# Kernel optimization log

Hardware: AMD Instinct MI355X
Metric: run time of the kernel (lower is better)

Reference implementation:

```python
import jax, jax.numpy as jnp
import numpy as np

DIM = 1024
HEADS = 16
HEAD_DIM = DIM // HEADS


def setup_inputs() -> dict:
    key = jax.random.key(0)
    ks = jax.random.split(key, 9)
    s = 1.0 / np.sqrt(DIM)
    return {
        "x": jax.random.normal(ks[0], (2, 2048, DIM), dtype=jnp.float32),
        "Wq": jax.random.normal(ks[1], (DIM, DIM), dtype=jnp.float32) * s,
        "bq": jnp.zeros((DIM,), dtype=jnp.float32),
        "Wk": jax.random.normal(ks[2], (DIM, DIM), dtype=jnp.float32) * s,
        "bk": jnp.zeros((DIM,), dtype=jnp.float32),
        "Wv": jax.random.normal(ks[3], (DIM, DIM), dtype=jnp.float32) * s,
        "bv": jnp.zeros((DIM,), dtype=jnp.float32),
        "Wo": jax.random.normal(ks[4], (DIM, DIM), dtype=jnp.float32) * s,
        "bo": jnp.zeros((DIM,), dtype=jnp.float32),
    }


def reference(x, Wq, bq, Wk, bk, Wv, bv, Wo, bo):
    B, S, D = x.shape
    H, Dh = HEADS, HEAD_DIM

    def split_heads(t):  # (B,S,D) -> (B,H,S,Dh)
        return t.reshape(B, S, H, Dh).transpose(0, 2, 1, 3)

    q = split_heads(x @ Wq + bq)
    k = split_heads(x @ Wk + bk)
    v = split_heads(x @ Wv + bv)

    scores = jnp.einsum("bhsd,bhtd->bhst", q, k) / np.sqrt(Dh).astype(x.dtype)
    attn = jax.nn.softmax(scores, axis=-1)
    ctx = jnp.einsum("bhst,bhtd->bhsd", attn, v)
    ctx = ctx.transpose(0, 2, 1, 3).reshape(B, S, D)
    return ctx @ Wo + bo
```

## Files before the change

kernel.cpp:

```cpp
#include <hip/hip_runtime.h>
#include <hip/hip_bf16.h>
#include <cstdint>

typedef __bf16 bf16;
typedef __bf16 bf16x8 __attribute__((ext_vector_type(8)));
typedef float f32x4 __attribute__((ext_vector_type(4)));
typedef float f32x8 __attribute__((ext_vector_type(8)));
typedef float f32x16 __attribute__((ext_vector_type(16)));

#define DIM   1024
#define SEQ   2048
#define BATCH 2
#define HEADS 16
#define HDIM  64

#define QSCALE 0.1803368801111204f

__device__ __forceinline__ void gload_lds16(const void* g, void* l) {
    __builtin_amdgcn_global_load_lds(
        (const __attribute__((address_space(1))) void*)g,
        (__attribute__((address_space(3))) void*)l,
        16, 0, 0);
}

__device__ __forceinline__ uint32_t pkbf(float a, float b) {
    union { bf16 h[2]; uint32_t u; } t;
    t.h[0] = (bf16)a; t.h[1] = (bf16)b;
    return t.u;
}

#define LO8(v)  __builtin_shufflevector(v, v, 0, 1, 2, 3, 4, 5, 6, 7)
#define HI8(v)  __builtin_shufflevector(v, v, 8, 9, 10, 11, 12, 13, 14, 15)
#define LO4(v)  __builtin_shufflevector(v, v, 0, 1, 2, 3)
#define HI4(v)  __builtin_shufflevector(v, v, 4, 5, 6, 7)

__global__ __launch_bounds__(256) void cvt_wt_kernel(const float* __restrict__ Wq,
                                                     const float* __restrict__ Wk,
                                                     const float* __restrict__ Wv,
                                                     const float* __restrict__ Wo,
                                                     bf16* __restrict__ Wt) {
    int z = blockIdx.z;
    const float* W = (z == 0) ? Wq : (z == 1) ? Wk : (z == 2) ? Wv : Wo;
    bf16* out = Wt + (size_t)z * DIM * DIM;
    int w = threadIdx.x >> 6, lane = threadIdx.x & 63;
    int n  = blockIdx.x * 64 + lane;
    int kb = blockIdx.y * 32 + w * 8;
    bf16x8 o;
#pragma unroll
    for (int j = 0; j < 8; ++j)
        o[j] = (bf16)W[(size_t)(kb + j) * DIM + n];
    *(bf16x8*)(out + (size_t)n * DIM + kb) = o;
}

template <int MODE>
__global__ __launch_bounds__(256) void gemm128_kernel(
        const void* __restrict__ Ap,
        const void* __restrict__ A2p,
        const float* __restrict__ lb,
        const bf16* __restrict__ WtB,
        const float* __restrict__ b0,
        const float* __restrict__ b1,
        const float* __restrict__ b2,
        void* __restrict__ outp) {
    constexpr int K = DIM;
    int z = (MODE == 0) ? blockIdx.z : 0;
    const bf16* Bt = WtB + (size_t)z * DIM * DIM;
    const float* bias = (MODE == 0) ? ((z == 0) ? b0 : (z == 1) ? b1 : b2) : b0;

    int m0 = blockIdx.y * 128, n0 = blockIdx.x * 128;
    int tid = threadIdx.x;
    int w = tid >> 6, lane = tid & 63, l15 = lane & 15, l4 = lane >> 4;
    int wr = (w >> 1) * 64, wc = (w & 1) * 64;

    __shared__ __align__(16) bf16 As[128 * 32];
    __shared__ __align__(16) bf16 Bs[128 * 32];

    int arow = tid >> 1, acol = (tid & 1) * 16;
    int r = m0 + arow;
    const float* asrc = (MODE == 0)
        ? (const float*)Ap + (size_t)r * K + acol : nullptr;

    f32x4 acc[4][4] = {};

    for (int k0 = 0; k0 < K; k0 += 32) {
#pragma unroll
        for (int rr = 0; rr < 2; ++rr) {
            int c = rr * 256 + tid;
            gload_lds16(Bt + (size_t)(n0 + (c >> 2)) * K + k0 + (c & 3) * 8, &Bs[c * 8]);
        }
        if constexpr (MODE == 0) {
            const float4* s4 = (const float4*)(asrc + k0);
            float4 f0 = s4[0], f1 = s4[1], f2 = s4[2], f3 = s4[3];
            bf16x8 e0, e1;
            e0[0] = (bf16)f0.x; e0[1] = (bf16)f0.y; e0[2] = (bf16)f0.z; e0[3] = (bf16)f0.w;
            e0[4] = (bf16)f1.x; e0[5] = (bf16)f1.y; e0[6] = (bf16)f1.z; e0[7] = (bf16)f1.w;
            e1[0] = (bf16)f2.x; e1[1] = (bf16)f2.y; e1[2] = (bf16)f2.z; e1[3] = (bf16)f2.w;
            e1[4] = (bf16)f3.x; e1[5] = (bf16)f3.y; e1[6] = (bf16)f3.z; e1[7] = (bf16)f3.w;
            *(bf16x8*)&As[arow * 32 + acol]     = e0;
            *(bf16x8*)&As[arow * 32 + acol + 8] = e1;
        } else {
            int s = r & (SEQ - 1), bbq = r >> 11;
            int hb2 = bbq * HEADS + ((k0 + acol) >> 6);
            float linv = 1.0f / (lb[(size_t)hb2 * SEQ + s]
                               + lb[((size_t)BATCH * HEADS + hb2) * SEQ + s]);
            const bf16* p0 = (const bf16*)Ap  + (size_t)r * DIM + k0 + acol;
            const bf16* p1 = (const bf16*)A2p + (size_t)r * DIM + k0 + acol;
            bf16x8 u0 = *(const bf16x8*)p0, u1 = *(const bf16x8*)(p0 + 8);
            bf16x8 t0 = *(const bf16x8*)p1, t1 = *(const bf16x8*)(p1 + 8);
            bf16x8 e0, e1;
#pragma unroll
            for (int i2 = 0; i2 < 8; ++i2) {
                e0[i2] = (bf16)(((float)u0[i2] + (float)t0[i2]) * linv);
                e1[i2] = (bf16)(((float)u1[i2] + (float)t1[i2]) * linv);
            }
            *(bf16x8*)&As[arow * 32 + acol]     = e0;
            *(bf16x8*)&As[arow * 32 + acol + 8] = e1;
        }
        __syncthreads();
        bf16x8 af[4], bfr[4];
#pragma unroll
        for (int m = 0; m < 4; ++m)
            af[m] = *(const bf16x8*)&As[(wr + m * 16 + l15) * 32 + l4 * 8];
#pragma unroll
        for (int n = 0; n < 4; ++n)
            bfr[n] = *(const bf16x8*)&Bs[(wc + n * 16 + l15) * 32 + l4 * 8];
#pragma unroll
        for (int m = 0; m < 4; ++m)
#pragma unroll
            for (int n = 0; n < 4; ++n)
                acc[m][n] = __builtin_amdgcn_mfma_f32_16x16x32_bf16(
                    af[m], bfr[n], acc[m][n], 0, 0, 0);
        __syncthreads();
    }

    float oscale = (MODE == 0 && z == 0) ? QSCALE : 1.0f;
#pragma unroll
    for (int n = 0; n < 4; ++n) {
        int col = n0 + wc + n * 16 + l15;
        float bv = bias[col];
#pragma unroll
        for (int m = 0; m < 4; ++m) {
            int rowb = m0 + wr + m * 16 + l4 * 4;
            if (MODE == 1) {
                float* out = (float*)outp;
#pragma unroll
                for (int i = 0; i < 4; ++i)
                    out[(size_t)(rowb + i) * DIM + col] = acc[m][n][i] + bv;
            } else if (z == 0) {
                bf16* out = (bf16*)outp;
                int h = col >> 6, d = col & 63;
#pragma unroll
                for (int i = 0; i < 4; ++i) {
                    int row = rowb + i;
                    int bb = row >> 11, s = row & 2047;
                    out[(((size_t)(bb * HEADS + h)) * SEQ + s) * HDIM + d] =
                        (bf16)((acc[m][n][i] + bv) * oscale);
                }
            } else if (z == 1) {
                char* out = (char*)outp + (size_t)(BATCH * HEADS * SEQ * HDIM) * 2;
                int h = col >> 6, d = col & 63;
                int ks = d >> 4, lbase = ((d >> 3) & 1) * 32, e = d & 7;
#pragma unroll
                for (int i = 0; i < 4; ++i) {
                    int row = rowb + i;
                    int bb = row >> 11, s = row & 2047;
                    int hb2 = bb * HEADS + h;
                    size_t off = (size_t)(hb2 * 64 + (s >> 5)) * 4096
                                 + ks * 1024 + ((s & 31) + lbase) * 16 + e * 2;
                    *(bf16*)(out + off) = (bf16)(acc[m][n][i] + bv);
                }
            } else {
                char* out = (char*)outp + (size_t)2 * (BATCH * HEADS * SEQ * HDIM) * 2;
                int h = col >> 6, d = col & 63;
                int dblk = d >> 5;
                int bb = rowb >> 11, s0 = rowb & 2047;
                int hb2 = bb * HEADS + h;
                int lane2 = (d & 31) + 32 * ((s0 >> 3) & 1);
                size_t off = (size_t)(hb2 * 64 + (s0 >> 5)) * 4096
                             + (dblk * 2 + ((s0 >> 4) & 1)) * 1024
                             + lane2 * 16 + (s0 & 7) * 2;
                union { bf16 hh[4]; ushort4 v; } pk;
#pragma unroll
                for (int i = 0; i < 4; ++i) pk.hh[i] = (bf16)(acc[m][n][i] + bv);
                *(ushort4*)(out + off) = pk.v;
            }
        }
    }
}

__global__ __launch_bounds__(256) void attn_kernel(const bf16* __restrict__ Q,
                                                   const bf16* __restrict__ Kf,
                                                   const bf16* __restrict__ Vf,
                                                   bf16* __restrict__ op0,
                                                   bf16* __restrict__ op1,
                                                   float* __restrict__ lbuf) {
    int bid = blockIdx.x;
    int xcd = bid & 7, i = bid >> 3;
    int hb  = xcd * 4 + (i >> 4);
    int rem = i & 15;
    int q0  = (rem >> 1) * 256;
    int si  = rem & 1;
    int bb = hb >> 4, h = hb & 15;
    int tid = threadIdx.x, w = tid >> 6, lane = tid & 63;
    int l31 = lane & 31, hi = lane >> 5;

    const bf16* Qh = Q + (size_t)hb * SEQ * HDIM;
    const char* kj = (const char*)Kf + (size_t)(hb * 64 + si * 32) * 4096 + lane * 16;
    const char* vj = (const char*)Vf + (size_t)(hb * 64 + si * 32) * 4096 + lane * 16;

    int qrowA = q0 + w * 64 + l31;
    int qrowB = qrowA + 32;
    bf16x8 qfA[4], qfB[4];
#pragma unroll
    for (int ks = 0; ks < 4; ++ks) {
        qfA[ks] = *(const bf16x8*)&Qh[(size_t)qrowA * HDIM + ks * 16 + hi * 8];
        qfB[ks] = *(const bf16x8*)&Qh[(size_t)qrowB * HDIM + ks * 16 + hi * 8];
    }

    f32x16 oA0 = {}, oA1 = {}, oB0 = {}, oB1 = {};
    float lA = 0.f, lB = 0.f;

    for (int j = 0; j < 32; ++j) {
        bf16x8 k0 = *(const bf16x8*)(kj);
        bf16x8 k1 = *(const bf16x8*)(kj + 1024);
        bf16x8 k2 = *(const bf16x8*)(kj + 2048);
        bf16x8 k3 = *(const bf16x8*)(kj + 3072);
        kj += 4096;

        f32x16 sA = {}, sB = {};
        __builtin_amdgcn_s_setprio(1);
        sA = __builtin_amdgcn_mfma_f32_32x32x16_bf16(k0, qfA[0], sA, 0, 0, 0);
        sA = __builtin_amdgcn_mfma_f32_32x32x16_bf16(k1, qfA[1], sA, 0, 0, 0);
        sA = __builtin_amdgcn_mfma_f32_32x32x16_bf16(k2, qfA[2], sA, 0, 0, 0);
        sA = __builtin_amdgcn_mfma_f32_32x32x16_bf16(k3, qfA[3], sA, 0, 0, 0);
        sB = __builtin_amdgcn_mfma_f32_32x32x16_bf16(k0, qfB[0], sB, 0, 0, 0);
        sB = __builtin_amdgcn_mfma_f32_32x32x16_bf16(k1, qfB[1], sB, 0, 0, 0);
        sB = __builtin_amdgcn_mfma_f32_32x32x16_bf16(k2, qfB[2], sB, 0, 0, 0);
        sB = __builtin_amdgcn_mfma_f32_32x32x16_bf16(k3, qfB[3], sB, 0, 0, 0);
        __builtin_amdgcn_s_setprio(0);

        bf16x8 v0 = *(const bf16x8*)(vj);
        bf16x8 v1 = *(const bf16x8*)(vj + 1024);
        bf16x8 v2 = *(const bf16x8*)(vj + 2048);
        bf16x8 v3 = *(const bf16x8*)(vj + 3072);
        vj += 4096;

#pragma unroll
        for (int r = 0; r < 16; ++r)
            sA[r] = __builtin_amdgcn_exp2f(sA[r]);
        {
            f32x8 a8 = LO8(sA) + HI8(sA);
            f32x4 a4 = LO4(a8) + HI4(a8);
            lA += (a4[0] + a4[1]) + (a4[2] + a4[3]);
        }
        bf16x8 paA0, paA1;
        {
            uint32_t w0 = pkbf(sA[0], sA[1]), w1 = pkbf(sA[2], sA[3]);
            uint32_t w2 = pkbf(sA[4], sA[5]), w3 = pkbf(sA[6], sA[7]);
            asm("v_permlane32_swap_b32 %0, %1" : "+v"(w0), "+v"(w2));
            asm("v_permlane32_swap_b32 %0, %1" : "+v"(w1), "+v"(w3));
            union { uint32_t u[4]; bf16x8 v; } t2;
            t2.u[0] = w0; t2.u[1] = w1; t2.u[2] = w2; t2.u[3] = w3;
            paA0 = t2.v;
            uint32_t u0 = pkbf(sA[8], sA[9]),   u1 = pkbf(sA[10], sA[11]);
            uint32_t u2 = pkbf(sA[12], sA[13]), u3 = pkbf(sA[14], sA[15]);
            asm("v_permlane32_swap_b32 %0, %1" : "+v"(u0), "+v"(u2));
            asm("v_permlane32_swap_b32 %0, %1" : "+v"(u1), "+v"(u3));
            union { uint32_t u[4]; bf16x8 v; } t3;
            t3.u[0] = u0; t3.u[1] = u1; t3.u[2] = u2; t3.u[3] = u3;
            paA1 = t3.v;
        }
        __builtin_amdgcn_s_setprio(1);
        oA0 = __builtin_amdgcn_mfma_f32_32x32x16_bf16(v0, paA0, oA0, 0, 0, 0);
        oA0 = __builtin_amdgcn_mfma_f32_32x32x16_bf16(v1, paA1, oA0, 0, 0, 0);
        oA1 = __builtin_amdgcn_mfma_f32_32x32x16_bf16(v2, paA0, oA1, 0, 0, 0);
        oA1 = __builtin_amdgcn_mfma_f32_32x32x16_bf16(v3, paA1, oA1, 0, 0, 0);
        __builtin_amdgcn_s_setprio(0);

#pragma unroll
        for (int r = 0; r < 16; ++r)
            sB[r] = __builtin_amdgcn_exp2f(sB[r]);
        {
            f32x8 a8 = LO8(sB) + HI8(sB);
            f32x4 a4 = LO4(a8) + HI4(a8);
            lB += (a4[0] + a4[1]) + (a4[2] + a4[3]);
        }
        bf16x8 paB0, paB1;
        {
            uint32_t w0 = pkbf(sB[0], sB[1]), w1 = pkbf(sB[2], sB[3]);
            uint32_t w2 = pkbf(sB[4], sB[5]), w3 = pkbf(sB[6], sB[7]);
            asm("v_permlane32_swap_b32 %0, %1" : "+v"(w0), "+v"(w2));
            asm("v_permlane32_swap_b32 %0, %1" : "+v"(w1), "+v"(w3));
            union { uint32_t u[4]; bf16x8 v; } t2;
            t2.u[0] = w0; t2.u[1] = w1; t2.u[2] = w2; t2.u[3] = w3;
            paB0 = t2.v;
            uint32_t u0 = pkbf(sB[8], sB[9]),   u1 = pkbf(sB[10], sB[11]);
            uint32_t u2 = pkbf(sB[12], sB[13]), u3 = pkbf(sB[14], sB[15]);
            asm("v_permlane32_swap_b32 %0, %1" : "+v"(u0), "+v"(u2));
            asm("v_permlane32_swap_b32 %0, %1" : "+v"(u1), "+v"(u3));
            union { uint32_t u[4]; bf16x8 v; } t3;
            t3.u[0] = u0; t3.u[1] = u1; t3.u[2] = u2; t3.u[3] = u3;
            paB1 = t3.v;
        }
        __builtin_amdgcn_s_setprio(1);
        oB0 = __builtin_amdgcn_mfma_f32_32x32x16_bf16(v0, paB0, oB0, 0, 0, 0);
        oB0 = __builtin_amdgcn_mfma_f32_32x32x16_bf16(v1, paB1, oB0, 0, 0, 0);
        oB1 = __builtin_amdgcn_mfma_f32_32x32x16_bf16(v2, paB0, oB1, 0, 0, 0);
        oB1 = __builtin_amdgcn_mfma_f32_32x32x16_bf16(v3, paB1, oB1, 0, 0, 0);
        __builtin_amdgcn_s_setprio(0);
    }

    lA += __shfl_xor(lA, 32);
    lB += __shfl_xor(lB, 32);
    bf16* op = si ? op1 : op0;
    if (hi == 0) {
        lbuf[((size_t)si * BATCH * HEADS + hb) * SEQ + qrowA] = lA;
        lbuf[((size_t)si * BATCH * HEADS + hb) * SEQ + qrowB] = lB;
    }
    size_t baseA = ((size_t)bb * SEQ + qrowA) * DIM + h * HDIM;
    size_t baseB = ((size_t)bb * SEQ + qrowB) * DIM + h * HDIM;
#pragma unroll
    for (int g = 0; g < 4; ++g) {
        int dh0 = 8 * g + 4 * hi;
        union { bf16 hh[4]; ushort4 u; } a0, a1, b0, b1;
#pragma unroll
        for (int i = 0; i < 4; ++i) {
            a0.hh[i] = (bf16)oA0[4 * g + i];
            a1.hh[i] = (bf16)oA1[4 * g + i];
            b0.hh[i] = (bf16)oB0[4 * g + i];
            b1.hh[i] = (bf16)oB1[4 * g + i];
        }
        *(ushort4*)&op[baseA + dh0]      = a0.u;
        *(ushort4*)&op[baseA + 32 + dh0] = a1.u;
        *(ushort4*)&op[baseB + dh0]      = b0.u;
        *(ushort4*)&op[baseB + 32 + dh0] = b1.u;
    }
}

extern "C" void kernel_launch(void* const* d_in, const int* in_sizes, int n_in,
                              void* d_out, int out_size, void* d_ws, size_t ws_size,
                              hipStream_t stream) {
    const float* x  = (const float*)d_in[0];
    const float* Wq = (const float*)d_in[1];
    const float* bq = (const float*)d_in[2];
    const float* Wk = (const float*)d_in[3];
    const float* bk = (const float*)d_in[4];
    const float* Wv = (const float*)d_in[5];
    const float* bv = (const float*)d_in[6];
    const float* Wo = (const float*)d_in[7];
    const float* bo = (const float*)d_in[8];

    char* ws = (char*)d_ws;
    bf16*  op0  = (bf16*)ws;
    bf16*  Wt   = (bf16*)(ws + (8u  << 20));
    float* lbuf = (float*)(ws + (8u  << 20));
    bf16*  Qb   = (bf16*)(ws + (16u << 20));
    bf16*  Kf   = (bf16*)(ws + (24u << 20));
    bf16*  Vf   = (bf16*)(ws + (32u << 20));
    bf16*  op1  = (bf16*)(ws + (40u << 20));

    cvt_wt_kernel<<<dim3(16, 32, 4), 256, 0, stream>>>(Wq, Wk, Wv, Wo, Wt);
    gemm128_kernel<0><<<dim3(8, 32, 3), 256, 0, stream>>>(
        x, nullptr, nullptr, Wt, bq, bk, bv, (void*)Qb);
    attn_kernel<<<512, 256, 0, stream>>>(Qb, Kf, Vf, op0, op1, lbuf);
    gemm128_kernel<1><<<dim3(8, 32, 1), 256, 0, stream>>>(
        op0, op1, lbuf, Wt + (size_t)3 * DIM * DIM, bo, bo, bo, (void*)d_out);
}
```

Baseline: 149.5 us.

## Split attention KV range four ways and merge partials in separate kernel

The attention kernel is templated on the number of KV splits. When the workspace is large enough it launches twice as many blocks, each covering a quarter of the keys and writing its own partial output and row sum. A new elementwise merge kernel adds the partials and normalises them into a single bf16 context buffer. The output projection GEMM can then load its A operand straight into LDS with global_load_lds instead of combining and normalising partials itself. This trades an extra kernel launch and an extra pass over the partial buffers for more attention parallelism and a simpler GEMM prologue.

```diff
diff --git a/kernel.cpp b/kernel.cpp
--- a/kernel.cpp
+++ b/kernel.cpp
@@ -55,8 +55,6 @@
 template <int MODE>
 __global__ __launch_bounds__(256) void gemm128_kernel(
         const void* __restrict__ Ap,
-        const void* __restrict__ A2p,
-        const float* __restrict__ lb,
         const bf16* __restrict__ WtB,
         const float* __restrict__ b0,
         const float* __restrict__ b1,
@@ -76,9 +74,8 @@
     __shared__ __align__(16) bf16 Bs[128 * 32];
 
     int arow = tid >> 1, acol = (tid & 1) * 16;
-    int r = m0 + arow;
     const float* asrc = (MODE == 0)
-        ? (const float*)Ap + (size_t)r * K + acol : nullptr;
+        ? (const float*)Ap + (size_t)(m0 + arow) * K + acol : nullptr;
 
     f32x4 acc[4][4] = {};
 
@@ -99,22 +96,12 @@
             *(bf16x8*)&As[arow * 32 + acol]     = e0;
             *(bf16x8*)&As[arow * 32 + acol + 8] = e1;
         } else {
-            int s = r & (SEQ - 1), bbq = r >> 11;
-            int hb2 = bbq * HEADS + ((k0 + acol) >> 6);
-            float linv = 1.0f / (lb[(size_t)hb2 * SEQ + s]
-                               + lb[((size_t)BATCH * HEADS + hb2) * SEQ + s]);
-            const bf16* p0 = (const bf16*)Ap  + (size_t)r * DIM + k0 + acol;
-            const bf16* p1 = (const bf16*)A2p + (size_t)r * DIM + k0 + acol;
-            bf16x8 u0 = *(const bf16x8*)p0, u1 = *(const bf16x8*)(p0 + 8);
-            bf16x8 t0 = *(const bf16x8*)p1, t1 = *(const bf16x8*)(p1 + 8);
-            bf16x8 e0, e1;
-#pragma unroll
-            for (int i2 = 0; i2 < 8; ++i2) {
-                e0[i2] = (bf16)(((float)u0[i2] + (float)t0[i2]) * linv);
-                e1[i2] = (bf16)(((float)u1[i2] + (float)t1[i2]) * linv);
+            const bf16* A = (const bf16*)Ap;
+#pragma unroll
+            for (int rr = 0; rr < 2; ++rr) {
+                int c = rr * 256 + tid;
+                gload_lds16(A + (size_t)(m0 + (c >> 2)) * K + k0 + (c & 3) * 8, &As[c * 8]);
             }
-            *(bf16x8*)&As[arow * 32 + acol]     = e0;
-            *(bf16x8*)&As[arow * 32 + acol + 8] = e1;
         }
         __syncthreads();
         bf16x8 af[4], bfr[4];
@@ -188,25 +175,31 @@
     }
 }
 
+template <int NSPLIT>
 __global__ __launch_bounds__(256) void attn_kernel(const bf16* __restrict__ Q,
                                                    const bf16* __restrict__ Kf,
                                                    const bf16* __restrict__ Vf,
                                                    bf16* __restrict__ op0,
                                                    bf16* __restrict__ op1,
+                                                   bf16* __restrict__ op2,
+                                                   bf16* __restrict__ op3,
                                                    float* __restrict__ lbuf) {
+    constexpr int BPH = 8 * NSPLIT;
     int bid = blockIdx.x;
     int xcd = bid & 7, i = bid >> 3;
-    int hb  = xcd * 4 + (i >> 4);
-    int rem = i & 15;
-    int q0  = (rem >> 1) * 256;
-    int si  = rem & 1;
+    int hb  = xcd * 4 + i / BPH;
+    int rem = i % BPH;
+    int q0  = (rem / NSPLIT) * 256;
+    int si  = rem % NSPLIT;
     int bb = hb >> 4, h = hb & 15;
     int tid = threadIdx.x, w = tid >> 6, lane = tid & 63;
     int l31 = lane & 31, hi = lane >> 5;
 
     const bf16* Qh = Q + (size_t)hb * SEQ * HDIM;
-    const char* kj = (const char*)Kf + (size_t)(hb * 64 + si * 32) * 4096 + lane * 16;
-    const char* vj = (const char*)Vf + (size_t)(hb * 64 + si * 32) * 4096 + lane * 16;
+    const char* kj = (const char*)Kf
+        + (size_t)(hb * 64 + si * (64 / NSPLIT)) * 4096 + lane * 16;
+    const char* vj = (const char*)Vf
+        + (size_t)(hb * 64 + si * (64 / NSPLIT)) * 4096 + lane * 16;
 
     int qrowA = q0 + w * 64 + l31;
     int qrowB = qrowA + 32;
@@ -220,7 +213,8 @@
     f32x16 oA0 = {}, oA1 = {}, oB0 = {}, oB1 = {};
     float lA = 0.f, lB = 0.f;
 
-    for (int j = 0; j < 32; ++j) {
+    constexpr int NJ = SEQ / NSPLIT / 32;
+    for (int j = 0; j < NJ; ++j) {
         bf16x8 k0 = *(const bf16x8*)(kj);
         bf16x8 k1 = *(const bf16x8*)(kj + 1024);
         bf16x8 k2 = *(const bf16x8*)(kj + 2048);
@@ -312,7 +306,7 @@
 
     lA += __shfl_xor(lA, 32);
     lB += __shfl_xor(lB, 32);
-    bf16* op = si ? op1 : op0;
+    bf16* op = (si == 0) ? op0 : (si == 1) ? op1 : (si == 2) ? op2 : op3;
     if (hi == 0) {
         lbuf[((size_t)si * BATCH * HEADS + hb) * SEQ + qrowA] = lA;
         lbuf[((size_t)si * BATCH * HEADS + hb) * SEQ + qrowB] = lB;
@@ -324,17 +318,54 @@
         int dh0 = 8 * g + 4 * hi;
         union { bf16 hh[4]; ushort4 u; } a0, a1, b0, b1;
 #pragma unroll
-        for (int i = 0; i < 4; ++i) {
-            a0.hh[i] = (bf16)oA0[4 * g + i];
-            a1.hh[i] = (bf16)oA1[4 * g + i];
-            b0.hh[i] = (bf16)oB0[4 * g + i];
-            b1.hh[i] = (bf16)oB1[4 * g + i];
+        for (int i2 = 0; i2 < 4; ++i2) {
+            a0.hh[i2] = (bf16)oA0[4 * g + i2];
+            a1.hh[i2] = (bf16)oA1[4 * g + i2];
+            b0.hh[i2] = (bf16)oB0[4 * g + i2];
+            b1.hh[i2] = (bf16)oB1[4 * g + i2];
         }
         *(ushort4*)&op[baseA + dh0]      = a0.u;
         *(ushort4*)&op[baseA + 32 + dh0] = a1.u;
         *(ushort4*)&op[baseB + dh0]      = b0.u;
         *(ushort4*)&op[baseB + 32 + dh0] = b1.u;
     }
+}
+
+template <int NSPLIT>
+__global__ __launch_bounds__(256) void merge_kernel(const bf16* __restrict__ op0,
+                                                    const bf16* __restrict__ op1,
+                                                    const bf16* __restrict__ op2,
+                                                    const bf16* __restrict__ op3,
+                                                    const float* __restrict__ lbuf,
+                                                    bf16* __restrict__ ctx) {
+    int idx = blockIdx.x * 256 + threadIdx.x;
+    size_t e8 = (size_t)idx * 8;
+    int row = (int)(e8 >> 10);
+    int d   = (int)(e8 & 1023);
+    int h = d >> 6;
+    int bb = row >> 11, s = row & 2047;
+    int hb = bb * HEADS + h;
+    float lsum = lbuf[(size_t)hb * SEQ + s]
+               + lbuf[((size_t)BATCH * HEADS + hb) * SEQ + s];
+    if constexpr (NSPLIT == 4)
+        lsum += lbuf[((size_t)2 * BATCH * HEADS + hb) * SEQ + s]
+              + lbuf[((size_t)3 * BATCH * HEADS + hb) * SEQ + s];
+    float inv = 1.0f / lsum;
+    bf16x8 a = *(const bf16x8*)&op0[e8];
+    bf16x8 b = *(const bf16x8*)&op1[e8];
+    float acc[8];
+#pragma unroll
+    for (int i = 0; i < 8; ++i) acc[i] = (float)a[i] + (float)b[i];
+    if constexpr (NSPLIT == 4) {
+        bf16x8 c = *(const bf16x8*)&op2[e8];
+        bf16x8 dd = *(const bf16x8*)&op3[e8];
+#pragma unroll
+        for (int i = 0; i < 8; ++i) acc[i] += (float)c[i] + (float)dd[i];
+    }
+    bf16x8 o;
+#pragma unroll
+    for (int i = 0; i < 8; ++i) o[i] = (bf16)(acc[i] * inv);
+    *(bf16x8*)&ctx[e8] = o;
 }
 
 extern "C" void kernel_launch(void* const* d_in, const int* in_sizes, int n_in,
@@ -358,11 +389,21 @@
     bf16*  Kf   = (bf16*)(ws + (24u << 20));
     bf16*  Vf   = (bf16*)(ws + (32u << 20));
     bf16*  op1  = (bf16*)(ws + (40u << 20));
+    bf16*  op2  = (bf16*)(ws + (48u << 20));
+    bf16*  op3  = (bf16*)(ws + (56u << 20));
 
     cvt_wt_kernel<<<dim3(16, 32, 4), 256, 0, stream>>>(Wq, Wk, Wv, Wo, Wt);
     gemm128_kernel<0><<<dim3(8, 32, 3), 256, 0, stream>>>(
-        x, nullptr, nullptr, Wt, bq, bk, bv, (void*)Qb);
-    attn_kernel<<<512, 256, 0, stream>>>(Qb, Kf, Vf, op0, op1, lbuf);
+        x, Wt, bq, bk, bv, (void*)Qb);
+
+    if (ws_size >= (64ull << 20)) {
+        attn_kernel<4><<<1024, 256, 0, stream>>>(Qb, Kf, Vf, op0, op1, op2, op3, lbuf);
+        merge_kernel<4><<<2048, 256, 0, stream>>>(op0, op1, op2, op3, lbuf, op0);
+    } else {
+        attn_kernel<2><<<512, 256, 0, stream>>>(Qb, Kf, Vf, op0, op1, op1, op1, lbuf);
+        merge_kernel<2><<<2048, 256, 0, stream>>>(op0, op1, op0, op0, lbuf, op0);
+    }
+
     gemm128_kernel<1><<<dim3(8, 32, 1), 256, 0, stream>>>(
-        op0, op1, lbuf, Wt + (size_t)3 * DIM * DIM, bo, bo, bo, (void*)d_out);
-}
+        op0, Wt + (size_t)3 * DIM * DIM, bo, bo, bo, (void*)d_out);
+}
```

Measured after the change: 140.8 us. 1.06x faster.
